# Optimization experiments

Measured on AMD Instinct MI355X. Metric: run time of the kernel, lower is better.

The kernel has to match this reference:

```python
import jax, jax.numpy as jnp
import numpy as np

LN_EPS = 1e-5
MIN_MASK_SUM = 1e-6


def setup_inputs() -> dict:
    key = jax.random.key(0)
    ks = jax.random.split(key, 8)
    B, N, D = 8, 576, 1024
    K, H, W = 64, 512, 512
    OUT, GEOM = 256, 5
    feature_map = jax.random.normal(ks[0], (B, N, D), dtype=jnp.float32)
    masks = jax.random.randint(ks[1], (B, K, H, W), 0, 2).astype(bool)
    s = 0.02
    w1 = jax.random.normal(ks[2], (D + GEOM, OUT), dtype=jnp.float32) * s
    b1 = jnp.zeros((OUT,), dtype=jnp.float32)
    ln_g = jnp.ones((OUT,), dtype=jnp.float32)
    ln_b = jnp.zeros((OUT,), dtype=jnp.float32)
    w2 = jax.random.normal(ks[3], (OUT, OUT), dtype=jnp.float32) * s
    b2 = jnp.zeros((OUT,), dtype=jnp.float32)
    return {"feature_map": feature_map, "masks": masks, "w1": w1, "b1": b1,
            "ln_g": ln_g, "ln_b": ln_b, "w2": w2, "b2": b2}


def _geom(masks):
    # masks: [B,K,H,W] bool -> [B,K,5] (cx, cy, area_norm, bbox_w, bbox_h)
    B, K, H, W = masks.shape
    mf = masks.astype(jnp.float32)
    area = mf.sum((-2, -1))                                  # [B,K]
    xg = jnp.arange(W, dtype=jnp.float32)
    yg = jnp.arange(H, dtype=jnp.float32)
    safe = jnp.maximum(area, 1.0)
    cx = jnp.einsum('bkhw,w->bk', mf, xg) / safe / W
    cy = jnp.einsum('bkhw,h->bk', mf, yg) / safe / H
    xs_any = masks.any(axis=2)                               # [B,K,W]
    ys_any = masks.any(axis=3)                               # [B,K,H]
    xi = jnp.arange(W, dtype=jnp.int32)
    yi = jnp.arange(H, dtype=jnp.int32)
    BIG = jnp.int32(1 << 30)
    xmin = jnp.min(jnp.where(xs_any, xi, BIG), -1)
    xmax = jnp.max(jnp.where(xs_any, xi, -1), -1)
    ymin = jnp.min(jnp.where(ys_any, yi, BIG), -1)
    ymax = jnp.max(jnp.where(ys_any, yi, -1), -1)
    bw = (xmax - xmin + 1).astype(jnp.float32) / W
    bh = (ymax - ymin + 1).astype(jnp.float32) / H
    geom = jnp.stack([cx, cy, area / (H * W), bw, bh], -1)   # [B,K,5]
    return jnp.where((area >= 1.0)[..., None], geom, 0.0)


def reference(feature_map, masks, w1, b1, ln_g, ln_b, w2, b2):
    B, N, D = feature_map.shape
    _, K, H, W = masks.shape
    Hf = int(round(N ** 0.5))
    # nearest-neighbor downsample of masks to the patch grid (torch 'nearest')
    ri = (jnp.arange(Hf) * H) // Hf
    ci = (jnp.arange(Hf) * W) // Hf
    m_small = masks[:, :, ri][:, :, :, ci].astype(jnp.float32).reshape(B, K, -1)  # [B,K,N]
    msum = jnp.maximum(m_small.sum(-1, keepdims=True), MIN_MASK_SUM)
    pooled = jnp.einsum('bkn,bnd->bkd', m_small, feature_map) / msum              # [B,K,D]
    pooled = pooled - feature_map.mean(axis=1, keepdims=True)                     # bg subtract
    geom = _geom(masks)                                                           # [B,K,5]
    x = jnp.concatenate([pooled, geom], axis=-1)                                  # [B,K,D+5]
    h = jax.nn.gelu(x @ w1 + b1, approximate=False)
    mu = h.mean(-1, keepdims=True)
    var = jnp.mean((h - mu) ** 2, axis=-1, keepdims=True)
    h = (h - mu) * jax.lax.rsqrt(var + LN_EPS) * ln_g + ln_b
    return h @ w2 + b2                                                            # [B,K,out]
```

## Files before the change

kernel.cpp:

```cpp
#include <hip/hip_runtime.h>
#include <math.h>

#define BB 8
#define NN 576
#define DD 1024
#define KK 64
#define HH 512
#define WW 512
#define OUTD 256
#define HF 24
#define XSTRIDE 1032

typedef int iv4 __attribute__((ext_vector_type(4)));

__global__ __launch_bounds__(576) void k_ms(const int* __restrict__ masks,
                                            float* __restrict__ msbuf,
                                            float* __restrict__ invbuf) {
    int bk = blockIdx.x;
    int tid = threadIdx.x;
    const int* mb = masks + (size_t)bk * (HH * WW);
    int i = tid / HF, j = tid - i * HF;
    int ri = (i * HH) / HF, ci = (j * WW) / HF;
    float v = (mb[ri * WW + ci] != 0) ? 1.f : 0.f;
    msbuf[(size_t)bk * NN + tid] = v;

    float s = v;
    for (int off = 32; off > 0; off >>= 1) s += __shfl_down(s, off);
    __shared__ float rsum[9];
    if ((tid & 63) == 0) rsum[tid >> 6] = s;
    __syncthreads();
    if (tid == 0) {
        float t = 0.f;
        for (int q = 0; q < 9; ++q) t += rsum[q];
        invbuf[bk] = 1.0f / fmaxf(t, 1e-6f);
    }
}

__global__ __launch_bounds__(512, 4) void k_fused(const int* __restrict__ masks,
                                                  const float* __restrict__ fm,
                                                  const float* __restrict__ msbuf,
                                                  const float* __restrict__ invbuf,
                                                  float* __restrict__ xbuf) {
    const int bid = blockIdx.x;
    const int tid = threadIdx.x;
    const int trio = bid / 3;
    const int rem = bid - trio * 3;

    __shared__ float fmT[2][32][68];
    __shared__ float mskS[2][64][68];
    __shared__ float fredL[64][32];
    __shared__ float pacc[256][12];
    __shared__ float fmean_s[32];
    __shared__ int r0[8], r1[8], r2[8], r3[8], r4[8], r5[8], r6[8];

    if (rem < 2) {
        const int bk = trio * 2 + rem;
        const iv4* mp = (const iv4*)(masks + (size_t)bk * (HH * WW));
        const int y0 = tid >> 7;
        const int xb = (tid & 127) << 2;
        int cnt = 0, w3a = 0, syr = 0, colany = 0;
        int ymn_it = 1 << 20, ymx_it = -1;

        #pragma unroll 8
        for (int it = 0; it < 128; ++it) {
            iv4 m = __builtin_nontemporal_load(&mp[tid + (it << 9)]);
            int sum4 = m.x + m.y + m.z + m.w;
            int mask4 = m.x | (m.y << 1) | (m.z << 2) | (m.w << 3);
            cnt += sum4;
            w3a += m.y + (m.z << 1) + ((m.w << 1) + m.w);
            syr += sum4 * it;
            colany |= mask4;
            if (mask4) { ymn_it = min(ymn_it, it); ymx_it = it; }
        }

        int sx = xb * cnt + w3a;
        int sy = (syr << 2) + y0 * cnt;
        int xmn = colany ? xb + __builtin_ctz((unsigned)colany) : (1 << 30);
        int xmx = colany ? xb + (31 - __builtin_clz((unsigned)colany)) : -1;
        int ymn = (ymx_it >= 0) ? (ymn_it << 2) + y0 : (1 << 30);
        int ymx = (ymx_it >= 0) ? (ymx_it << 2) + y0 : -1;

        for (int off = 32; off > 0; off >>= 1) {
            cnt += __shfl_down(cnt, off);
            sx  += __shfl_down(sx,  off);
            sy  += __shfl_down(sy,  off);
            xmn = min(xmn, __shfl_down(xmn, off));
            xmx = max(xmx, __shfl_down(xmx, off));
            ymn = min(ymn, __shfl_down(ymn, off));
            ymx = max(ymx, __shfl_down(ymx, off));
        }
        int wv = tid >> 6;
        if ((tid & 63) == 0) {
            r0[wv] = cnt; r1[wv] = sx; r2[wv] = sy;
            r3[wv] = xmn; r4[wv] = xmx; r5[wv] = ymn; r6[wv] = ymx;
        }
        __syncthreads();
        if (tid == 0) {
            for (int i = 1; i < 8; ++i) {
                cnt += r0[i]; sx += r1[i]; sy += r2[i];
                xmn = min(xmn, r3[i]); xmx = max(xmx, r4[i]);
                ymn = min(ymn, r5[i]); ymx = max(ymx, r6[i]);
            }
            float* gp = xbuf + (size_t)bk * XSTRIDE + DD;
            if (cnt >= 1) {
                float area = (float)cnt;
                gp[0] = (float)sx / area * (1.0f / 512.0f);
                gp[1] = (float)sy / area * (1.0f / 512.0f);
                gp[2] = area * (1.0f / 262144.0f);
                gp[3] = (float)(xmx - xmn + 1) * (1.0f / 512.0f);
                gp[4] = (float)(ymx - ymn + 1) * (1.0f / 512.0f);
            } else {
                gp[0] = 0.f; gp[1] = 0.f; gp[2] = 0.f; gp[3] = 0.f; gp[4] = 0.f;
            }
            gp[5] = 0.f; gp[6] = 0.f; gp[7] = 0.f;
        }
    } else {
        const int b = bid & 7;
        const int dt = trio >> 3;
        const int d0 = dt << 5;
        const int team = tid >> 8, ttid = tid & 255;
        const int kg = ttid >> 4, dg = ttid & 15;
        const int frow = tid >> 3, fc4 = (tid & 7) << 2;
        const int mk = tid >> 3, mf = tid & 7;

        float acc[4][2] = {{0.f,0.f},{0.f,0.f},{0.f,0.f},{0.f,0.f}};
        float facc4[4] = {0.f, 0.f, 0.f, 0.f};

        const float* fmb = fm + (size_t)b * NN * DD + d0;
        const float* msb = msbuf + (size_t)b * KK * NN;

        for (int r = 0; r < 5; ++r) {
            {
                int n0 = r << 6;
                float4 v = *(const float4*)&fmb[(size_t)(n0 + frow) * DD + fc4];
                facc4[0] += v.x; facc4[1] += v.y; facc4[2] += v.z; facc4[3] += v.w;
                fmT[0][fc4 + 0][frow] = v.x;
                fmT[0][fc4 + 1][frow] = v.y;
                fmT[0][fc4 + 2][frow] = v.z;
                fmT[0][fc4 + 3][frow] = v.w;
                float4 a = *(const float4*)&msb[(size_t)mk * NN + n0 + (mf << 2)];
                float4 c = *(const float4*)&msb[(size_t)mk * NN + n0 + ((mf + 8) << 2)];
                *(float4*)&mskS[0][mk][(mf << 2)] = a;
                *(float4*)&mskS[0][mk][((mf + 8) << 2)] = c;
            }
            if (r < 4) {
                int n0 = (5 + r) << 6;
                float4 v = *(const float4*)&fmb[(size_t)(n0 + frow) * DD + fc4];
                facc4[0] += v.x; facc4[1] += v.y; facc4[2] += v.z; facc4[3] += v.w;
                fmT[1][fc4 + 0][frow] = v.x;
                fmT[1][fc4 + 1][frow] = v.y;
                fmT[1][fc4 + 2][frow] = v.z;
                fmT[1][fc4 + 3][frow] = v.w;
                float4 a = *(const float4*)&msb[(size_t)mk * NN + n0 + (mf << 2)];
                float4 c = *(const float4*)&msb[(size_t)mk * NN + n0 + ((mf + 8) << 2)];
                *(float4*)&mskS[1][mk][(mf << 2)] = a;
                *(float4*)&mskS[1][mk][((mf + 8) << 2)] = c;
            }
            __syncthreads();
            int c = (team == 0) ? r : 5 + r;
            if (c < 9) {
                #pragma unroll 4
                for (int q = 0; q < 16; ++q) {
                    float4 fa = *(const float4*)&fmT[team][dg][q << 2];
                    float4 fb = *(const float4*)&fmT[team][dg + 16][q << 2];
                    #pragma unroll
                    for (int kk = 0; kk < 4; ++kk) {
                        float4 mv = *(const float4*)&mskS[team][(kg << 2) + kk][q << 2];
                        acc[kk][0] += mv.x * fa.x + mv.y * fa.y + mv.z * fa.z + mv.w * fa.w;
                        acc[kk][1] += mv.x * fb.x + mv.y * fb.y + mv.z * fb.z + mv.w * fb.w;
                    }
                }
            }
            __syncthreads();
        }

        fredL[frow][fc4 + 0] = facc4[0];
        fredL[frow][fc4 + 1] = facc4[1];
        fredL[frow][fc4 + 2] = facc4[2];
        fredL[frow][fc4 + 3] = facc4[3];
        if (team == 1) {
            #pragma unroll
            for (int kk = 0; kk < 4; ++kk) {
                pacc[ttid][kk * 2 + 0] = acc[kk][0];
                pacc[ttid][kk * 2 + 1] = acc[kk][1];
            }
        }
        __syncthreads();
        if (tid < 32) {
            float s = 0.f;
            #pragma unroll
            for (int i = 0; i < 64; ++i) s += fredL[i][tid];
            fmean_s[tid] = s * (1.0f / 576.0f);
        }
        __syncthreads();
        if (team == 0) {
            float fm_a = fmean_s[dg], fm_b = fmean_s[dg + 16];
            #pragma unroll
            for (int kk = 0; kk < 4; ++kk) {
                int k = kg * 4 + kk;
                float inv = invbuf[b * KK + k];
                float* xp = xbuf + (size_t)(b * KK + k) * XSTRIDE + d0;
                xp[dg]      = (acc[kk][0] + pacc[ttid][kk * 2 + 0]) * inv - fm_a;
                xp[dg + 16] = (acc[kk][1] + pacc[ttid][kk * 2 + 1]) * inv - fm_b;
            }
        }
    }
}

__global__ __launch_bounds__(512) void k_mlp(const float* __restrict__ xbuf,
                                             const float* __restrict__ w1,
                                             const float* __restrict__ b1,
                                             const float* __restrict__ ln_g,
                                             const float* __restrict__ ln_b,
                                             const float* __restrict__ w2,
                                             const float* __restrict__ b2,
                                             float* __restrict__ out) {
    int row0 = blockIdx.x * 4;
    int tid = threadIdx.x;
    int w = tid >> 6, lane = tid & 63;
    int c4 = lane * 4;
    int col = tid & 255, rhalf = tid >> 8;

    __shared__ float xs[4][XSTRIDE];
    __shared__ float hp[8][4][OUTD];
    __shared__ float hs[4][OUTD];

    for (int i = tid; i < 4 * (XSTRIDE / 4); i += 512) {
        int r = i / (XSTRIDE / 4), cq = i % (XSTRIDE / 4);
        *(float4*)&xs[r][cq * 4] =
            *(const float4*)&xbuf[(size_t)(row0 + r) * XSTRIDE + cq * 4];
    }
    __syncthreads();

    float acc[4][4] = {};
    int js = w * 128;
    int je = (w == 7) ? 1029 : js + 128;
    int j = js;
    for (; j + 4 <= je; j += 4) {
        float4 xv0 = *(const float4*)&xs[0][j];
        float4 xv1 = *(const float4*)&xs[1][j];
        float4 xv2 = *(const float4*)&xs[2][j];
        float4 xv3 = *(const float4*)&xs[3][j];
#define STEPA(jj, X0, X1, X2, X3)                                              \
        {                                                                      \
            float4 wv = *(const float4*)&w1[(size_t)(j + jj) * OUTD + c4];     \
            acc[0][0] += X0 * wv.x; acc[0][1] += X0 * wv.y;                    \
            acc[0][2] += X0 * wv.z; acc[0][3] += X0 * wv.w;                    \
            acc[1][0] += X1 * wv.x; acc[1][1] += X1 * wv.y;                    \
            acc[1][2] += X1 * wv.z; acc[1][3] += X1 * wv.w;                    \
            acc[2][0] += X2 * wv.x; acc[2][1] += X2 * wv.y;                    \
            acc[2][2] += X2 * wv.z; acc[2][3] += X2 * wv.w;                    \
            acc[3][0] += X3 * wv.x; acc[3][1] += X3 * wv.y;                    \
            acc[3][2] += X3 * wv.z; acc[3][3] += X3 * wv.w;                    \
        }
        STEPA(0, xv0.x, xv1.x, xv2.x, xv3.x)
        STEPA(1, xv0.y, xv1.y, xv2.y, xv3.y)
        STEPA(2, xv0.z, xv1.z, xv2.z, xv3.z)
        STEPA(3, xv0.w, xv1.w, xv2.w, xv3.w)
    }
    for (; j < je; ++j) {
        float xv[4] = {xs[0][j], xs[1][j], xs[2][j], xs[3][j]};
        #pragma unroll
        for (int ci = 0; ci < 4; ++ci) {
            float wvv = w1[(size_t)j * OUTD + c4 + ci];
            #pragma unroll
            for (int r = 0; r < 4; ++r) acc[r][ci] += xv[r] * wvv;
        }
    }
    #pragma unroll
    for (int r = 0; r < 4; ++r)
        *(float4*)&hp[w][r][c4] = make_float4(acc[r][0], acc[r][1], acc[r][2], acc[r][3]);
    __syncthreads();

    float h2[2];
    float b1v = b1[col];
    #pragma unroll
    for (int r2 = 0; r2 < 2; ++r2) {
        int r = rhalf * 2 + r2;
        float sv = b1v;
        #pragma unroll
        for (int ww = 0; ww < 8; ++ww) sv += hp[ww][r][col];
        h2[r2] = 0.5f * sv * (1.0f + erff(sv * 0.70710678118654752f));
    }
    __shared__ float s1[8][2], s2[8][2];
    #pragma unroll
    for (int r2 = 0; r2 < 2; ++r2) {
        float a = h2[r2], qv = h2[r2] * h2[r2];
        for (int off = 32; off > 0; off >>= 1) {
            a += __shfl_down(a, off);
            qv += __shfl_down(qv, off);
        }
        if (lane == 0) { s1[w][r2] = a; s2[w][r2] = qv; }
    }
    __syncthreads();
    __shared__ float mu_[4], rsd_[4];
    if (tid < 4) {
        int rh = tid >> 1, r2 = tid & 1;
        float a = 0.f, qv = 0.f;
        #pragma unroll
        for (int i = 0; i < 4; ++i) {
            a += s1[rh * 4 + i][r2];
            qv += s2[rh * 4 + i][r2];
        }
        float mu = a * (1.0f / 256.0f);
        float var = qv * (1.0f / 256.0f) - mu * mu;
        mu_[tid] = mu;
        rsd_[tid] = rsqrtf(var + 1e-5f);
    }
    __syncthreads();
    float gv = ln_g[col], bv = ln_b[col];
    #pragma unroll
    for (int r2 = 0; r2 < 2; ++r2) {
        int r = rhalf * 2 + r2;
        hs[r][col] = (h2[r2] - mu_[r]) * rsd_[r] * gv + bv;
    }
    __syncthreads();

    float a2[4][4] = {};
    int j2 = w * 32;
    for (int g = 0; g < 8; ++g, j2 += 4) {
        float4 h0 = *(const float4*)&hs[0][j2];
        float4 h1 = *(const float4*)&hs[1][j2];
        float4 h2v = *(const float4*)&hs[2][j2];
        float4 h3 = *(const float4*)&hs[3][j2];
#define STEPB(jj, X0, X1, X2, X3)                                              \
        {                                                                      \
            float4 wv = *(const float4*)&w2[(size_t)(j2 + jj) * OUTD + c4];    \
            a2[0][0] += X0 * wv.x; a2[0][1] += X0 * wv.y;                      \
            a2[0][2] += X0 * wv.z; a2[0][3] += X0 * wv.w;                      \
            a2[1][0] += X1 * wv.x; a2[1][1] += X1 * wv.y;                      \
            a2[1][2] += X1 * wv.z; a2[1][3] += X1 * wv.w;                      \
            a2[2][0] += X2 * wv.x; a2[2][1] += X2 * wv.y;                      \
            a2[2][2] += X2 * wv.z; a2[2][3] += X2 * wv.w;                      \
            a2[3][0] += X3 * wv.x; a2[3][1] += X3 * wv.y;                      \
            a2[3][2] += X3 * wv.z; a2[3][3] += X3 * wv.w;                      \
        }
        STEPB(0, h0.x, h1.x, h2v.x, h3.x)
        STEPB(1, h0.y, h1.y, h2v.y, h3.y)
        STEPB(2, h0.z, h1.z, h2v.z, h3.z)
        STEPB(3, h0.w, h1.w, h2v.w, h3.w)
    }
    #pragma unroll
    for (int r = 0; r < 4; ++r)
        *(float4*)&hp[w][r][c4] = make_float4(a2[r][0], a2[r][1], a2[r][2], a2[r][3]);
    __syncthreads();

    float b2v = b2[col];
    #pragma unroll
    for (int r2 = 0; r2 < 2; ++r2) {
        int r = rhalf * 2 + r2;
        float o = b2v;
        #pragma unroll
        for (int ww = 0; ww < 8; ++ww) o += hp[ww][r][col];
        out[(size_t)(row0 + r) * OUTD + col] = o;
    }
}

extern "C" void kernel_launch(void* const* d_in, const int* in_sizes, int n_in,
                              void* d_out, int out_size, void* d_ws, size_t ws_size,
                              hipStream_t stream) {
    const float* fm    = (const float*)d_in[0];
    const int*   masks = (const int*)d_in[1];
    const float* w1    = (const float*)d_in[2];
    const float* b1    = (const float*)d_in[3];
    const float* ln_g  = (const float*)d_in[4];
    const float* ln_b  = (const float*)d_in[5];
    const float* w2    = (const float*)d_in[6];
    const float* b2    = (const float*)d_in[7];
    float* out = (float*)d_out;

    float* msbuf  = (float*)d_ws;
    float* invbuf = msbuf + 512 * NN;
    float* xbuf   = invbuf + 512;

    k_ms   <<<512, 576, 0, stream>>>(masks, msbuf, invbuf);
    k_fused<<<768, 512, 0, stream>>>(masks, fm, msbuf, invbuf, xbuf);
    k_mlp  <<<128, 512, 0, stream>>>(xbuf, w1, b1, ln_g, ln_b, w2, b2, out);
}
```

Measured before the change: 125.1 us.

## Merge mask geometry into downsample kernel and split pooling into its own kernel

Mask geometry reduction (area, centroid, bbox) moves out of the heterogeneous fused kernel into the mask-downsample kernel, which now runs 1024-thread blocks that each scan a full mask. Pooling becomes a standalone kernel with 256 blocks. This drops one pass of block-level work dispatching and gives the bandwidth-bound 512 MB mask scan its own kernel with more threads per mask. The trade-off is that geometry work no longer overlaps with the pooling blocks in the same launch, which serializes the two phases.

```diff
diff --git a/kernel.cpp b/kernel.cpp
--- a/kernel.cpp
+++ b/kernel.cpp
@@ -13,196 +13,194 @@
 
 typedef int iv4 __attribute__((ext_vector_type(4)));
 
-__global__ __launch_bounds__(576) void k_ms(const int* __restrict__ masks,
-                                            float* __restrict__ msbuf,
-                                            float* __restrict__ invbuf) {
+__global__ __launch_bounds__(1024) void k_geom(const int* __restrict__ masks,
+                                               float* __restrict__ msbuf,
+                                               float* __restrict__ invbuf,
+                                               float* __restrict__ xbuf) {
     int bk = blockIdx.x;
     int tid = threadIdx.x;
     const int* mb = masks + (size_t)bk * (HH * WW);
-    int i = tid / HF, j = tid - i * HF;
-    int ri = (i * HH) / HF, ci = (j * WW) / HF;
-    float v = (mb[ri * WW + ci] != 0) ? 1.f : 0.f;
-    msbuf[(size_t)bk * NN + tid] = v;
-
-    float s = v;
-    for (int off = 32; off > 0; off >>= 1) s += __shfl_down(s, off);
-    __shared__ float rsum[9];
-    if ((tid & 63) == 0) rsum[tid >> 6] = s;
+    const iv4* mp = (const iv4*)mb;
+
+    __shared__ float rsum[16];
+    __shared__ int r0[16], r1[16], r2[16], r3[16], r4[16], r5[16], r6[16];
+
+    float msv = 0.f;
+    if (tid < NN) {
+        int i = tid / HF, j = tid - i * HF;
+        int ri = (i * HH) / HF, ci = (j * WW) / HF;
+        msv = (mb[ri * WW + ci] != 0) ? 1.f : 0.f;
+    }
+
+    const int y0 = tid >> 7;
+    const int xb = (tid & 127) << 2;
+    int cnt = 0, w3a = 0, syr = 0, colany = 0;
+    int ymn_it = 1 << 20, ymx_it = -1;
+
+    #pragma unroll 8
+    for (int it = 0; it < 64; ++it) {
+        iv4 m = __builtin_nontemporal_load(&mp[tid + (it << 10)]);
+        int sum4 = m.x + m.y + m.z + m.w;
+        int mask4 = m.x | (m.y << 1) | (m.z << 2) | (m.w << 3);
+        cnt += sum4;
+        w3a += m.y + (m.z << 1) + ((m.w << 1) + m.w);
+        syr += sum4 * it;
+        colany |= mask4;
+        if (mask4) { ymn_it = min(ymn_it, it); ymx_it = it; }
+    }
+
+    int sx = xb * cnt + w3a;
+    int sy = (syr << 3) + y0 * cnt;
+    int xmn = colany ? xb + __builtin_ctz((unsigned)colany) : (1 << 30);
+    int xmx = colany ? xb + (31 - __builtin_clz((unsigned)colany)) : -1;
+    int ymn = (ymx_it >= 0) ? (ymn_it << 3) + y0 : (1 << 30);
+    int ymx = (ymx_it >= 0) ? (ymx_it << 3) + y0 : -1;
+
+    for (int off = 32; off > 0; off >>= 1) {
+        cnt += __shfl_down(cnt, off);
+        sx  += __shfl_down(sx,  off);
+        sy  += __shfl_down(sy,  off);
+        xmn = min(xmn, __shfl_down(xmn, off));
+        xmx = max(xmx, __shfl_down(xmx, off));
+        ymn = min(ymn, __shfl_down(ymn, off));
+        ymx = max(ymx, __shfl_down(ymx, off));
+    }
+    int wv = tid >> 6;
+    if ((tid & 63) == 0) {
+        r0[wv] = cnt; r1[wv] = sx; r2[wv] = sy;
+        r3[wv] = xmn; r4[wv] = xmx; r5[wv] = ymn; r6[wv] = ymx;
+    }
+    {
+        float v = msv;
+        for (int off = 32; off > 0; off >>= 1) v += __shfl_down(v, off);
+        if ((tid & 63) == 0) rsum[wv] = v;
+    }
     __syncthreads();
     if (tid == 0) {
-        float t = 0.f;
-        for (int q = 0; q < 9; ++q) t += rsum[q];
-        invbuf[bk] = 1.0f / fmaxf(t, 1e-6f);
-    }
+        for (int i = 1; i < 16; ++i) {
+            cnt += r0[i]; sx += r1[i]; sy += r2[i];
+            xmn = min(xmn, r3[i]); xmx = max(xmx, r4[i]);
+            ymn = min(ymn, r5[i]); ymx = max(ymx, r6[i]);
+        }
+        float* gp = xbuf + (size_t)bk * XSTRIDE + DD;
+        if (cnt >= 1) {
+            float area = (float)cnt;
+            gp[0] = (float)sx / area * (1.0f / 512.0f);
+            gp[1] = (float)sy / area * (1.0f / 512.0f);
+            gp[2] = area * (1.0f / 262144.0f);
+            gp[3] = (float)(xmx - xmn + 1) * (1.0f / 512.0f);
+            gp[4] = (float)(ymx - ymn + 1) * (1.0f / 512.0f);
+        } else {
+            gp[0] = 0.f; gp[1] = 0.f; gp[2] = 0.f; gp[3] = 0.f; gp[4] = 0.f;
+        }
+        gp[5] = 0.f; gp[6] = 0.f; gp[7] = 0.f;
+
+        float s = 0.f;
+        for (int i = 0; i < 16; ++i) s += rsum[i];
+        invbuf[bk] = 1.0f / fmaxf(s, 1e-6f);
+    }
+    if (tid < NN) msbuf[(size_t)bk * NN + tid] = msv;
 }
 
-__global__ __launch_bounds__(512, 4) void k_fused(const int* __restrict__ masks,
-                                                  const float* __restrict__ fm,
-                                                  const float* __restrict__ msbuf,
-                                                  const float* __restrict__ invbuf,
-                                                  float* __restrict__ xbuf) {
+__global__ __launch_bounds__(512) void k_pool(const float* __restrict__ fm,
+                                              const float* __restrict__ msbuf,
+                                              const float* __restrict__ invbuf,
+                                              float* __restrict__ xbuf) {
     const int bid = blockIdx.x;
+    const int b = bid & 7;
+    const int dt = bid >> 3;
+    const int d0 = dt << 5;
     const int tid = threadIdx.x;
-    const int trio = bid / 3;
-    const int rem = bid - trio * 3;
+    const int team = tid >> 8, ttid = tid & 255;
+    const int kg = ttid >> 4, dg = ttid & 15;
+    const int frow = tid >> 3, fc4 = (tid & 7) << 2;
+    const int mk = tid >> 3, mf = tid & 7;
 
     __shared__ float fmT[2][32][68];
     __shared__ float mskS[2][64][68];
     __shared__ float fredL[64][32];
     __shared__ float pacc[256][12];
     __shared__ float fmean_s[32];
-    __shared__ int r0[8], r1[8], r2[8], r3[8], r4[8], r5[8], r6[8];
-
-    if (rem < 2) {
-        const int bk = trio * 2 + rem;
-        const iv4* mp = (const iv4*)(masks + (size_t)bk * (HH * WW));
-        const int y0 = tid >> 7;
-        const int xb = (tid & 127) << 2;
-        int cnt = 0, w3a = 0, syr = 0, colany = 0;
-        int ymn_it = 1 << 20, ymx_it = -1;
-
-        #pragma unroll 8
-        for (int it = 0; it < 128; ++it) {
-            iv4 m = __builtin_nontemporal_load(&mp[tid + (it << 9)]);
-            int sum4 = m.x + m.y + m.z + m.w;
-            int mask4 = m.x | (m.y << 1) | (m.z << 2) | (m.w << 3);
-            cnt += sum4;
-            w3a += m.y + (m.z << 1) + ((m.w << 1) + m.w);
-            syr += sum4 * it;
-            colany |= mask4;
-            if (mask4) { ymn_it = min(ymn_it, it); ymx_it = it; }
-        }
-
-        int sx = xb * cnt + w3a;
-        int sy = (syr << 2) + y0 * cnt;
-        int xmn = colany ? xb + __builtin_ctz((unsigned)colany) : (1 << 30);
-        int xmx = colany ? xb + (31 - __builtin_clz((unsigned)colany)) : -1;
-        int ymn = (ymx_it >= 0) ? (ymn_it << 2) + y0 : (1 << 30);
-        int ymx = (ymx_it >= 0) ? (ymx_it << 2) + y0 : -1;
-
-        for (int off = 32; off > 0; off >>= 1) {
-            cnt += __shfl_down(cnt, off);
-            sx  += __shfl_down(sx,  off);
-            sy  += __shfl_down(sy,  off);
-            xmn = min(xmn, __shfl_down(xmn, off));
-            xmx = max(xmx, __shfl_down(xmx, off));
-            ymn = min(ymn, __shfl_down(ymn, off));
-            ymx = max(ymx, __shfl_down(ymx, off));
-        }
-        int wv = tid >> 6;
-        if ((tid & 63) == 0) {
-            r0[wv] = cnt; r1[wv] = sx; r2[wv] = sy;
-            r3[wv] = xmn; r4[wv] = xmx; r5[wv] = ymn; r6[wv] = ymx;
+
+    float acc[4][2] = {{0.f,0.f},{0.f,0.f},{0.f,0.f},{0.f,0.f}};
+    float facc4[4] = {0.f, 0.f, 0.f, 0.f};
+
+    const float* fmb = fm + (size_t)b * NN * DD + d0;
+    const float* msb = msbuf + (size_t)b * KK * NN;
+
+    for (int r = 0; r < 5; ++r) {
+        {
+            int n0 = r << 6;
+            float4 v = *(const float4*)&fmb[(size_t)(n0 + frow) * DD + fc4];
+            facc4[0] += v.x; facc4[1] += v.y; facc4[2] += v.z; facc4[3] += v.w;
+            fmT[0][fc4 + 0][frow] = v.x;
+            fmT[0][fc4 + 1][frow] = v.y;
+            fmT[0][fc4 + 2][frow] = v.z;
+            fmT[0][fc4 + 3][frow] = v.w;
+            float4 a = *(const float4*)&msb[(size_t)mk * NN + n0 + (mf << 2)];
+            float4 c = *(const float4*)&msb[(size_t)mk * NN + n0 + ((mf + 8) << 2)];
+            *(float4*)&mskS[0][mk][(mf << 2)] = a;
+            *(float4*)&mskS[0][mk][((mf + 8) << 2)] = c;
+        }
+        if (r < 4) {
+            int n0 = (5 + r) << 6;
+            float4 v = *(const float4*)&fmb[(size_t)(n0 + frow) * DD + fc4];
+            facc4[0] += v.x; facc4[1] += v.y; facc4[2] += v.z; facc4[3] += v.w;
+            fmT[1][fc4 + 0][frow] = v.x;
+            fmT[1][fc4 + 1][frow] = v.y;
+            fmT[1][fc4 + 2][frow] = v.z;
+            fmT[1][fc4 + 3][frow] = v.w;
+            float4 a = *(const float4*)&msb[(size_t)mk * NN + n0 + (mf << 2)];
+            float4 c = *(const float4*)&msb[(size_t)mk * NN + n0 + ((mf + 8) << 2)];
+            *(float4*)&mskS[1][mk][(mf << 2)] = a;
+            *(float4*)&mskS[1][mk][((mf + 8) << 2)] = c;
         }
         __syncthreads();
-        if (tid == 0) {
-            for (int i = 1; i < 8; ++i) {
-                cnt += r0[i]; sx += r1[i]; sy += r2[i];
-                xmn = min(xmn, r3[i]); xmx = max(xmx, r4[i]);
-                ymn = min(ymn, r5[i]); ymx = max(ymx, r6[i]);
-            }
-            float* gp = xbuf + (size_t)bk * XSTRIDE + DD;
-            if (cnt >= 1) {
-                float area = (float)cnt;
-                gp[0] = (float)sx / area * (1.0f / 512.0f);
-                gp[1] = (float)sy / area * (1.0f / 512.0f);
-                gp[2] = area * (1.0f / 262144.0f);
-                gp[3] = (float)(xmx - xmn + 1) * (1.0f / 512.0f);
-                gp[4] = (float)(ymx - ymn + 1) * (1.0f / 512.0f);
-            } else {
-                gp[0] = 0.f; gp[1] = 0.f; gp[2] = 0.f; gp[3] = 0.f; gp[4] = 0.f;
-            }
-            gp[5] = 0.f; gp[6] = 0.f; gp[7] = 0.f;
-        }
-    } else {
-        const int b = bid & 7;
-        const int dt = trio >> 3;
-        const int d0 = dt << 5;
-        const int team = tid >> 8, ttid = tid & 255;
-        const int kg = ttid >> 4, dg = ttid & 15;
-        const int frow = tid >> 3, fc4 = (tid & 7) << 2;
-        const int mk = tid >> 3, mf = tid & 7;
-
-        float acc[4][2] = {{0.f,0.f},{0.f,0.f},{0.f,0.f},{0.f,0.f}};
-        float facc4[4] = {0.f, 0.f, 0.f, 0.f};
-
-        const float* fmb = fm + (size_t)b * NN * DD + d0;
-        const float* msb = msbuf + (size_t)b * KK * NN;
-
-        for (int r = 0; r < 5; ++r) {
-            {
-                int n0 = r << 6;
-                float4 v = *(const float4*)&fmb[(size_t)(n0 + frow) * DD + fc4];
-                facc4[0] += v.x; facc4[1] += v.y; facc4[2] += v.z; facc4[3] += v.w;
-                fmT[0][fc4 + 0][frow] = v.x;
-                fmT[0][fc4 + 1][frow] = v.y;
-                fmT[0][fc4 + 2][frow] = v.z;
-                fmT[0][fc4 + 3][frow] = v.w;
-                float4 a = *(const float4*)&msb[(size_t)mk * NN + n0 + (mf << 2)];
-                float4 c = *(const float4*)&msb[(size_t)mk * NN + n0 + ((mf + 8) << 2)];
-                *(float4*)&mskS[0][mk][(mf << 2)] = a;
-                *(float4*)&mskS[0][mk][((mf + 8) << 2)] = c;
-            }
-            if (r < 4) {
-                int n0 = (5 + r) << 6;
-                float4 v = *(const float4*)&fmb[(size_t)(n0 + frow) * DD + fc4];
-                facc4[0] += v.x; facc4[1] += v.y; facc4[2] += v.z; facc4[3] += v.w;
-                fmT[1][fc4 + 0][frow] = v.x;
-                fmT[1][fc4 + 1][frow] = v.y;
-                fmT[1][fc4 + 2][frow] = v.z;
-                fmT[1][fc4 + 3][frow] = v.w;
-                float4 a = *(const float4*)&msb[(size_t)mk * NN + n0 + (mf << 2)];
-                float4 c = *(const float4*)&msb[(size_t)mk * NN + n0 + ((mf + 8) << 2)];
-                *(float4*)&mskS[1][mk][(mf << 2)] = a;
-                *(float4*)&mskS[1][mk][((mf + 8) << 2)] = c;
-            }
-            __syncthreads();
-            int c = (team == 0) ? r : 5 + r;
-            if (c < 9) {
-                #pragma unroll 4
-                for (int q = 0; q < 16; ++q) {
-                    float4 fa = *(const float4*)&fmT[team][dg][q << 2];
-                    float4 fb = *(const float4*)&fmT[team][dg + 16][q << 2];
-                    #pragma unroll
-                    for (int kk = 0; kk < 4; ++kk) {
-                        float4 mv = *(const float4*)&mskS[team][(kg << 2) + kk][q << 2];
-                        acc[kk][0] += mv.x * fa.x + mv.y * fa.y + mv.z * fa.z + mv.w * fa.w;
-                        acc[kk][1] += mv.x * fb.x + mv.y * fb.y + mv.z * fb.z + mv.w * fb.w;
-                    }
+        int c = (team == 0) ? r : 5 + r;
+        if (c < 9) {
+            #pragma unroll 4
+            for (int q = 0; q < 16; ++q) {
+                float4 fa = *(const float4*)&fmT[team][dg][q << 2];
+                float4 fb = *(const float4*)&fmT[team][dg + 16][q << 2];
+                #pragma unroll
+                for (int kk = 0; kk < 4; ++kk) {
+                    float4 mv = *(const float4*)&mskS[team][(kg << 2) + kk][q << 2];
+                    acc[kk][0] += mv.x * fa.x + mv.y * fa.y + mv.z * fa.z + mv.w * fa.w;
+                    acc[kk][1] += mv.x * fb.x + mv.y * fb.y + mv.z * fb.z + mv.w * fb.w;
                 }
             }
-            __syncthreads();
-        }
-
-        fredL[frow][fc4 + 0] = facc4[0];
-        fredL[frow][fc4 + 1] = facc4[1];
-        fredL[frow][fc4 + 2] = facc4[2];
-        fredL[frow][fc4 + 3] = facc4[3];
-        if (team == 1) {
-            #pragma unroll
-            for (int kk = 0; kk < 4; ++kk) {
-                pacc[ttid][kk * 2 + 0] = acc[kk][0];
-                pacc[ttid][kk * 2 + 1] = acc[kk][1];
-            }
         }
         __syncthreads();
-        if (tid < 32) {
-            float s = 0.f;
-            #pragma unroll
-            for (int i = 0; i < 64; ++i) s += fredL[i][tid];
-            fmean_s[tid] = s * (1.0f / 576.0f);
-        }
-        __syncthreads();
-        if (team == 0) {
-            float fm_a = fmean_s[dg], fm_b = fmean_s[dg + 16];
-            #pragma unroll
-            for (int kk = 0; kk < 4; ++kk) {
-                int k = kg * 4 + kk;
-                float inv = invbuf[b * KK + k];
-                float* xp = xbuf + (size_t)(b * KK + k) * XSTRIDE + d0;
-                xp[dg]      = (acc[kk][0] + pacc[ttid][kk * 2 + 0]) * inv - fm_a;
-                xp[dg + 16] = (acc[kk][1] + pacc[ttid][kk * 2 + 1]) * inv - fm_b;
-            }
+    }
+
+    fredL[frow][fc4 + 0] = facc4[0];
+    fredL[frow][fc4 + 1] = facc4[1];
+    fredL[frow][fc4 + 2] = facc4[2];
+    fredL[frow][fc4 + 3] = facc4[3];
+    if (team == 1) {
+        #pragma unroll
+        for (int kk = 0; kk < 4; ++kk) {
+            pacc[ttid][kk * 2 + 0] = acc[kk][0];
+            pacc[ttid][kk * 2 + 1] = acc[kk][1];
+        }
+    }
+    __syncthreads();
+    if (tid < 32) {
+        float s = 0.f;
+        #pragma unroll
+        for (int i = 0; i < 64; ++i) s += fredL[i][tid];
+        fmean_s[tid] = s * (1.0f / 576.0f);
+    }
+    __syncthreads();
+    if (team == 0) {
+        float fm_a = fmean_s[dg], fm_b = fmean_s[dg + 16];
+        #pragma unroll
+        for (int kk = 0; kk < 4; ++kk) {
+            int k = kg * 4 + kk;
+            float inv = invbuf[b * KK + k];
+            float* xp = xbuf + (size_t)(b * KK + k) * XSTRIDE + d0;
+            xp[dg]      = (acc[kk][0] + pacc[ttid][kk * 2 + 0]) * inv - fm_a;
+            xp[dg + 16] = (acc[kk][1] + pacc[ttid][kk * 2 + 1]) * inv - fm_b;
         }
     }
 }
@@ -373,7 +371,7 @@
     float* invbuf = msbuf + 512 * NN;
     float* xbuf   = invbuf + 512;
 
-    k_ms   <<<512, 576, 0, stream>>>(masks, msbuf, invbuf);
-    k_fused<<<768, 512, 0, stream>>>(masks, fm, msbuf, invbuf, xbuf);
-    k_mlp  <<<128, 512, 0, stream>>>(xbuf, w1, b1, ln_g, ln_b, w2, b2, out);
+    k_geom<<<512, 1024, 0, stream>>>(masks, msbuf, invbuf, xbuf);
+    k_pool<<<256, 512, 0, stream>>>(fm, msbuf, invbuf, xbuf);
+    k_mlp <<<128, 512, 0, stream>>>(xbuf, w1, b1, ln_g, ln_b, w2, b2, out);
 }
```

After: 130.6 us. 4.4% more time.
